# Optimization experiments

Measured on AMD Instinct MI355X. Metric: run time of the kernel, lower is better.

## Reference

```python
import jax, jax.numpy as jnp
import numpy as np

B, N, D, DEPTH = 1, 512, 128, 4


def mlp_apply(W, x):
    # W: (depth, d, d), x: (..., d). First layer has no activation, then silu before each matmul.
    x = x @ W[0]
    for i in range(1, DEPTH):
        x = jax.nn.silu(x) @ W[i]
    return x


def _binop(x, y):
    # linear recurrence combine: s_t = a_t * s_{t-1} + b_t
    a1, b1 = x
    a2, b2 = y
    return (a1 * a2, a2 * b1 + b2)


def setup_inputs() -> dict:
    key = jax.random.key(0)
    ks = jax.random.split(key, 7)
    s = 0.02  # scale for projection weights (torch Linear-like init magnitude)
    return {
        "seq": jax.random.normal(ks[0], (B, N, D), jnp.float32),
        "W_mem": jax.random.normal(ks[1], (DEPTH, D, D), jnp.float32) * (D ** -0.5),
        "W_q": jax.random.normal(ks[2], (D, D), jnp.float32) * s,
        "W_kv": jax.random.normal(ks[3], (D, 2 * D), jnp.float32) * s,
        "W_mom": jax.random.normal(ks[4], (D, 1), jnp.float32) * s,
        "W_step": jax.random.normal(ks[5], (D, 1), jnp.float32) * s,
        "W_decay": jax.random.normal(ks[6], (D, 1), jnp.float32) * s,
    }


def reference(seq, W_mem, W_q, W_kv, W_mom, W_step, W_decay):
    b, n, d = seq.shape
    # --- store_memories ---
    adaptive_lr = (seq @ W_step)[..., 0]            # (b, n)
    adaptive_mom = seq @ W_mom                      # (b, n, 1)
    decay = jax.nn.sigmoid(seq @ W_decay)           # (b, n, 1)

    kv = seq.reshape(b * n, d) @ W_kv               # (bn, 2d)
    keys, values = kv[:, :d], kv[:, d:]

    def loss_fn(W, k, v):
        pred = mlp_apply(W, k)                      # (d,)
        # (pred - v)^2 .mean(-1).sum() for a single sample == mean over d
        return jnp.mean((pred - v) ** 2)

    # per-sample meta-gradients wrt memory MLP weights
    losses, grads = jax.vmap(jax.value_and_grad(loss_fn, argnums=0), in_axes=(None, 0, 0))(W_mem, keys, values)
    grads = grads.reshape(b, n, DEPTH, d, d)
    surprise = grads * (-adaptive_lr)[..., None, None, None]   # (b,n,depth,d,d)

    # momentum_t = adaptive_mom_t * momentum_{t-1} + surprise_t  (assoc. scan over n)
    am = adaptive_mom[..., None, None]              # (b, n, 1, 1, 1)
    _, momentum = jax.lax.associative_scan(_binop, (am, surprise), axis=1)

    # update_t = (1 - decay_t) * update_{t-1} + momentum_t
    dec = (1.0 - decay)[..., None, None]            # (b, n, 1, 1, 1)
    _, updates = jax.lax.associative_scan(_binop, (dec, momentum), axis=1)

    # --- retrieve_memories with per-token updated weights ---
    q = (seq @ W_q).reshape(b * n, d)
    W_tok = (W_mem[None, None] + updates).reshape(b * n, DEPTH, d, d)
    retrieved = jax.vmap(mlp_apply)(W_tok, q).reshape(b, n, d)
    return retrieved
```

## Files before the change

kernel.cpp:

```cpp
#include <hip/hip_runtime.h>
#include <hip/hip_bf16.h>
#include <math.h>

#define N 512
#define NN (N*N)
#define D 128
#define DD (D*D)
#define ND (N*D)
#define LSTR 132
#define CSTR 36

__device__ __forceinline__ float sigmoidf_(float x) { return 1.f / (1.f + expf(-x)); }

__global__ void k_transpose(const float* __restrict__ W_mem, float* __restrict__ WT) {
    int idx = blockIdx.x * 256 + threadIdx.x;
    int l = idx / DD;
    int r = idx % DD;
    int i = r / D;
    int j = r % D;
    WT[idx] = W_mem[(l + 1) * DD + j * D + i];
}

__global__ __launch_bounds__(512) void k_phase1(
    const float* __restrict__ seq, const float* __restrict__ W_mem,
    const float* __restrict__ W_q, const float* __restrict__ W_kv,
    const float* __restrict__ W_mom, const float* __restrict__ W_step,
    const float* __restrict__ W_decay, const float* __restrict__ WT,
    float* __restrict__ Q, float* __restrict__ INS, float* __restrict__ ES,
    float* __restrict__ am, float* __restrict__ dec)
{
    __shared__ float s_seq[D], s_v[D], s_cur[D];
    __shared__ float s_h[4][D];
    __shared__ float s_part[4][D];
    __shared__ float s_p3[4][3][D];
    __shared__ float s_red[8];
    __shared__ float s_lr;

    const int t = blockIdx.x;
    const int tid = threadIdx.x;
    const int j = tid & 127;
    const int p = tid >> 7;
    const int i0 = p * 32;

    if (p == 0) s_seq[j] = seq[t * D + j];
    __syncthreads();

    float ps = 0.f;
    if (p == 1) ps = s_seq[j] * W_step[j];
    else if (p == 2) ps = s_seq[j] * W_mom[j];
    else if (p == 3) ps = s_seq[j] * W_decay[j];
#pragma unroll
    for (int off = 32; off > 0; off >>= 1) ps += __shfl_down(ps, off);
    if ((tid & 63) == 0) s_red[tid >> 6] = ps;
    __syncthreads();
    if (tid == 0) s_lr = s_red[2] + s_red[3];
    else if (tid == 1) am[t] = s_red[4] + s_red[5];
    else if (tid == 2) dec[t] = 1.f - sigmoidf_(s_red[6] + s_red[7]);

    float kp = 0.f, vp = 0.f, qp = 0.f;
#pragma unroll 8
    for (int ii = 0; ii < 32; ii++) {
        int i = i0 + ii;
        float si = s_seq[i];
        kp += si * W_kv[i * 256 + j];
        vp += si * W_kv[i * 256 + 128 + j];
        qp += si * W_q[i * 128 + j];
    }
    s_p3[p][0][j] = kp; s_p3[p][1][j] = vp; s_p3[p][2][j] = qp;
    __syncthreads();
    if (p == 0) {
        float kj = s_p3[0][0][j] + s_p3[1][0][j] + s_p3[2][0][j] + s_p3[3][0][j];
        s_cur[j] = kj;
        INS[t * D + j] = kj;
    } else if (p == 1) {
        s_v[j] = s_p3[0][1][j] + s_p3[1][1][j] + s_p3[2][1][j] + s_p3[3][1][j];
    } else if (p == 2) {
        Q[t * D + j] = s_p3[0][2][j] + s_p3[1][2][j] + s_p3[2][2][j] + s_p3[3][2][j];
    }
    __syncthreads();

    for (int l = 0; l < 4; l++) {
        const float* Wl = W_mem + l * DD;
        float yp = 0.f;
#pragma unroll 8
        for (int ii = 0; ii < 32; ii++) {
            int i = i0 + ii;
            yp += s_cur[i] * Wl[i * D + j];
        }
        s_part[p][j] = yp;
        __syncthreads();
        if (p == 0) {
            float y = s_part[0][j] + s_part[1][j] + s_part[2][j] + s_part[3][j];
            s_h[l][j] = y;
            if (l < 3) {
                float a = y * sigmoidf_(y);
                s_cur[j] = a;
                INS[(l + 1) * ND + t * D + j] = a;
            }
        }
        __syncthreads();
    }

    if (p == 0) {
        float e = -s_lr * (2.f / (float)D) * (s_h[3][j] - s_v[j]);
        ES[3 * ND + t * D + j] = e;
        s_cur[j] = e;
    }
    __syncthreads();

    for (int l = 3; l >= 1; l--) {
        const float* Wt = WT + (l - 1) * DD;
        float gp = 0.f;
#pragma unroll 8
        for (int ii = 0; ii < 32; ii++) {
            int i = i0 + ii;
            gp += s_cur[i] * Wt[i * D + j];
        }
        s_part[p][j] = gp;
        __syncthreads();
        if (p == 0) {
            float g = s_part[0][j] + s_part[1][j] + s_part[2][j] + s_part[3][j];
            float h = s_h[l - 1][j];
            float sg = sigmoidf_(h);
            float e2 = g * (sg * (1.f + h * (1.f - sg)));
            ES[(l - 1) * ND + t * D + j] = e2;
            s_cur[j] = e2;
        }
        __syncthreads();
    }
}

__global__ __launch_bounds__(512) void k_logscan(
    const float* __restrict__ am, const float* __restrict__ dec,
    double* __restrict__ LA, double* __restrict__ LDp, int* __restrict__ NC)
{
    __shared__ double sa[N], sd[N];
    __shared__ int sn[N];
    const int t = threadIdx.x;
    float a = am[t];
    float d = dec[t];
    sa[t] = log((double)fmaxf(fabsf(a), 1e-38f));
    sd[t] = log((double)fmaxf(d, 1e-38f));
    sn[t] = (a < 0.f) ? 1 : 0;
    __syncthreads();
    for (int off = 1; off < N; off <<= 1) {
        double va = 0.0, vd = 0.0; int vn = 0;
        if (t >= off) { va = sa[t - off]; vd = sd[t - off]; vn = sn[t - off]; }
        __syncthreads();
        sa[t] += va; sd[t] += vd; sn[t] += vn;
        __syncthreads();
    }
    LA[t] = sa[t]; LDp[t] = sd[t]; NC[t] = sn[t];
}

__global__ __launch_bounds__(256) void k_build(
    const double* __restrict__ LA, const double* __restrict__ LDp,
    const int* __restrict__ NC,
    float* __restrict__ Amat, float* __restrict__ Dmat)
{
    int idx = blockIdx.x * 256 + threadIdx.x;
    int u = idx >> 9;
    int s = idx & (N - 1);
    float va = 0.f, vd = 0.f;
    if (s <= u) {
        va = expf((float)(LA[u] - LA[s]));
        if ((NC[u] - NC[s]) & 1) va = -va;
        vd = expf((float)(LDp[u] - LDp[s]));
    }
    Amat[idx] = va;
    Dmat[idx] = vd;
}

__global__ __launch_bounds__(256) void k_betamm(
    const float* __restrict__ Dmat, const float* __restrict__ Amat,
    float* __restrict__ betaP)
{
    const int bs = blockIdx.x;
    const int bt = blockIdx.y;
    const int z  = blockIdx.z;
    if (bs > bt) return;
    const int span = bt - bs + 1;
    const int chunk = (span + 3) >> 2;
    const int kBeg = bs + z * chunk;
    const int kEnd = (kBeg + chunk < bt + 1) ? (kBeg + chunk) : (bt + 1);
    if (kBeg >= kEnd) return;

    __shared__ float sA[32 * 34];
    __shared__ float sDT[32 * 34];

    const int tid = threadIdx.x;
    const int tx = tid & 15;
    const int ty = tid >> 4;
    float acc00 = 0.f, acc01 = 0.f, acc10 = 0.f, acc11 = 0.f;

    for (int kt = kBeg; kt < kEnd; kt++) {
        for (int i = tid; i < 1024; i += 256) {
            int r = i >> 5, c = i & 31;
            sA[r * 34 + c]  = Amat[(kt * 32 + r) * N + bs * 32 + c];
            sDT[c * 34 + r] = Dmat[(bt * 32 + r) * N + kt * 32 + c];
        }
        __syncthreads();
#pragma unroll 8
        for (int k = 0; k < 32; k++) {
            float2 a = *(float2*)&sA[k * 34 + 2 * tx];
            float2 d = *(float2*)&sDT[k * 34 + 2 * ty];
            acc00 += d.x * a.x; acc01 += d.x * a.y;
            acc10 += d.y * a.x; acc11 += d.y * a.y;
        }
        __syncthreads();
    }
    float* bp = betaP + z * NN + (bt * 32 + 2 * ty) * N + bs * 32 + 2 * tx;
    *(float2*)bp       = make_float2(acc00, acc01);
    *(float2*)(bp + N) = make_float2(acc10, acc11);
}

__global__ __launch_bounds__(256) void k_betared(
    const float* __restrict__ betaP, float* __restrict__ beta)
{
    int idx4 = blockIdx.x * 256 + threadIdx.x;
    int t  = idx4 >> 7;
    int s0 = (idx4 & 127) * 4;
    int bt = t >> 5, bs = s0 >> 5;
    float4 v = make_float4(0.f, 0.f, 0.f, 0.f);
    if (bs <= bt) {
        int span = bt - bs + 1;
        int chunk = (span + 3) >> 2;
        int nz = (span + chunk - 1) / chunk;
        v = *(const float4*)(betaP + t * N + s0);
        for (int z = 1; z < nz; z++) {
            float4 u = *(const float4*)(betaP + z * NN + t * N + s0);
            v.x += u.x; v.y += u.y; v.z += u.z; v.w += u.w;
        }
    }
    *(float4*)(beta + t * N + s0) = v;
}

__global__ __launch_bounds__(256) void k_layer(
    const float* __restrict__ Xsrc, float* __restrict__ Pout,
    const float* __restrict__ Wl, const float* __restrict__ INSl,
    const float* __restrict__ ESl, const float* __restrict__ beta,
    int mode)
{
    const int r = blockIdx.x;
    const int z = blockIdx.y;
    const bool isW = (z == 8);
    if (!isW && 4 * z > r) return;
    const int t0 = r * 16;
    const int lane = threadIdx.x;

    __shared__ float sX[16 * LSTR];
    __shared__ float sI[32 * LSTR];
    __shared__ float sE[32 * LSTR];
    __shared__ float sc[16 * CSTR];

    const int nzs = (r >> 2) + 1;
#pragma unroll
    for (int i = 0; i < 2; i++) {
        int f4 = lane + 256 * i;
        int row = f4 >> 5, c4 = f4 & 31;
        float4 v = ((const float4*)(Xsrc + t0 * D))[f4];
        if (mode) {
            for (int zz = 1; zz < nzs; zz++) {
                float4 u = ((const float4*)(Xsrc + zz * ND + t0 * D))[f4];
                v.x += u.x; v.y += u.y; v.z += u.z; v.w += u.w;
            }
            float4 w = ((const float4*)(Xsrc + 8 * ND + t0 * D))[f4];
            v.x += w.x; v.y += w.y; v.z += w.z; v.w += w.w;
            v.x = v.x * sigmoidf_(v.x); v.y = v.y * sigmoidf_(v.y);
            v.z = v.z * sigmoidf_(v.z); v.w = v.w * sigmoidf_(v.w);
        }
        *(float4*)(sX + row * LSTR + c4 * 4) = v;
    }

    const int ti  = lane >> 4;
    const int q15 = lane & 15;
    const int j8  = q15 * 8;

    if (isW) {
        __syncthreads();
        float acc[8];
#pragma unroll
        for (int b = 0; b < 8; b++) acc[b] = 0.f;
#pragma unroll 4
        for (int k = 0; k < D; k++) {
            float4 w0 = *(const float4*)(Wl + k * D + j8);
            float4 w1 = *(const float4*)(Wl + k * D + j8 + 4);
            float xv = sX[ti * LSTR + k];
            acc[0] += xv * w0.x; acc[1] += xv * w0.y;
            acc[2] += xv * w0.z; acc[3] += xv * w0.w;
            acc[4] += xv * w1.x; acc[5] += xv * w1.y;
            acc[6] += xv * w1.z; acc[7] += xv * w1.w;
        }
        float* yp = Pout + 8 * ND + (t0 + ti) * D + j8;
        *(float4*)yp       = make_float4(acc[0], acc[1], acc[2], acc[3]);
        *(float4*)(yp + 4) = make_float4(acc[4], acc[5], acc[6], acc[7]);
        return;
    }

    const int si0 = q15 * 2;
    float acc[8];
#pragma unroll
    for (int b = 0; b < 8; b++) acc[b] = 0.f;

    for (int sub = 0; sub < 2; sub++) {
        const int s0 = z * 64 + sub * 32;
        __syncthreads();
#pragma unroll
        for (int i = 0; i < 4; i++) {
            int f4 = lane + 256 * i;
            int row = f4 >> 5, c4 = f4 & 31;
            float4 a = ((const float4*)(INSl + s0 * D))[f4];
            float4 b = ((const float4*)(ESl + s0 * D))[f4];
            *(float4*)(sI + row * LSTR + c4 * 4) = a;
            *(float4*)(sE + row * LSTR + c4 * 4) = b;
        }
        float b0 = beta[(t0 + ti) * N + s0 + si0];
        float b1 = beta[(t0 + ti) * N + s0 + si0 + 1];
        __syncthreads();

        float g0 = 0.f, g1 = 0.f;
#pragma unroll 8
        for (int k4 = 0; k4 < D; k4 += 4) {
            float4 a  = *(float4*)(sX + ti * LSTR + k4);
            float4 p0 = *(float4*)(sI + si0 * LSTR + k4);
            float4 p1 = *(float4*)(sI + (si0 + 1) * LSTR + k4);
            g0 += a.x * p0.x + a.y * p0.y + a.z * p0.z + a.w * p0.w;
            g1 += a.x * p1.x + a.y * p1.y + a.z * p1.z + a.w * p1.w;
        }
        sc[ti * CSTR + si0]     = g0 * b0;
        sc[ti * CSTR + si0 + 1] = g1 * b1;
        __syncthreads();

#pragma unroll 8
        for (int s = 0; s < 32; s++) {
            float cv = sc[ti * CSTR + s];
            float4 e0 = *(float4*)(sE + s * LSTR + j8);
            float4 e1 = *(float4*)(sE + s * LSTR + j8 + 4);
            acc[0] += cv * e0.x; acc[1] += cv * e0.y;
            acc[2] += cv * e0.z; acc[3] += cv * e0.w;
            acc[4] += cv * e1.x; acc[5] += cv * e1.y;
            acc[6] += cv * e1.z; acc[7] += cv * e1.w;
        }
    }

    float* yp = Pout + z * ND + (t0 + ti) * D + j8;
    *(float4*)yp       = make_float4(acc[0], acc[1], acc[2], acc[3]);
    *(float4*)(yp + 4) = make_float4(acc[4], acc[5], acc[6], acc[7]);
}

__global__ __launch_bounds__(256) void k_reduce(
    const float* __restrict__ P, float* __restrict__ out)
{
    int f4 = blockIdx.x * 256 + threadIdx.x;
    int t = f4 >> 5;
    int r = t >> 4;
    int nzs = (r >> 2) + 1;
    float4 v = ((const float4*)P)[f4];
    for (int zz = 1; zz < nzs; zz++) {
        float4 u = ((const float4*)(P + zz * ND))[f4];
        v.x += u.x; v.y += u.y; v.z += u.z; v.w += u.w;
    }
    float4 w = ((const float4*)(P + 8 * ND))[f4];
    v.x += w.x; v.y += w.y; v.z += w.z; v.w += w.w;
    ((float4*)out)[f4] = v;
}

extern "C" void kernel_launch(void* const* d_in, const int* in_sizes, int n_in,
                              void* d_out, int out_size, void* d_ws, size_t ws_size,
                              hipStream_t stream) {
    const float* seq     = (const float*)d_in[0];
    const float* W_mem   = (const float*)d_in[1];
    const float* W_q     = (const float*)d_in[2];
    const float* W_kv    = (const float*)d_in[3];
    const float* W_mom   = (const float*)d_in[4];
    const float* W_step  = (const float*)d_in[5];
    const float* W_decay = (const float*)d_in[6];
    float* out = (float*)d_out;

    float* ws   = (float*)d_ws;
    float* am   = ws;
    float* dec  = am + N;
    float* Q    = dec + N;
    float* INS  = Q + ND;
    float* ES   = INS + 4 * ND;
    float* beta = ES + 4 * ND;
    float* WT   = beta + NN;
    float* Amat = WT + 3 * DD;
    float* Dmat = Amat + NN;
    float* Pa   = Dmat + NN;
    float* Pb   = Pa + 9 * ND;
    double* LA  = (double*)(Pb + 9 * ND);
    double* LDp = LA + N;
    int* NC     = (int*)(LDp + N);
    float* betaP = Pa;

    k_transpose<<<192, 256, 0, stream>>>(W_mem, WT);
    k_phase1<<<N, 512, 0, stream>>>(seq, W_mem, W_q, W_kv, W_mom, W_step, W_decay,
                                    WT, Q, INS, ES, am, dec);
    k_logscan<<<1, N, 0, stream>>>(am, dec, LA, LDp, NC);
    k_build<<<(NN) / 256, 256, 0, stream>>>(LA, LDp, NC, Amat, Dmat);
    dim3 mmgrid(N / 32, N / 32, 4);
    k_betamm<<<mmgrid, 256, 0, stream>>>(Dmat, Amat, betaP);
    k_betared<<<NN / 4 / 256, 256, 0, stream>>>(betaP, beta);

    dim3 lgrid(32, 9);
    k_layer<<<lgrid, 256, 0, stream>>>(Q,  Pa, W_mem,          INS,          ES,          beta, 0);
    k_layer<<<lgrid, 256, 0, stream>>>(Pa, Pb, W_mem + DD,     INS + ND,     ES + ND,     beta, 1);
    k_layer<<<lgrid, 256, 0, stream>>>(Pb, Pa, W_mem + 2 * DD, INS + 2 * ND, ES + 2 * ND, beta, 1);
    k_layer<<<lgrid, 256, 0, stream>>>(Pa, Pb, W_mem + 3 * DD, INS + 3 * ND, ES + 3 * ND, beta, 1);
    k_reduce<<<64, 256, 0, stream>>>(Pb, out);
}
```

Measured before the change: 173.5 us.

## Fuse decay-matrix build into beta matmul, drop transpose, split layer s-range finer

Removes the separate transpose kernel by reading W_mem rows directly with float4 loads in the backward pass of phase1. The Amat/Dmat build kernel is fused into the beta matmul, which now computes the exp entries on the fly from the log-prefix sums, so the two N×N matrices are no longer written to and read back from memory. The layer kernel's source-token split goes from 8 slabs of 64 to 17 slabs of 32, which adds blocks for parallelism and removes the inner sub-loop. The cost is more partial-sum slabs for k_reduce and the next layer to read, and repeated exp evaluations inside the matmul tiles.

```diff
diff --git a/kernel.cpp b/kernel.cpp
--- a/kernel.cpp
+++ b/kernel.cpp
@@ -9,30 +9,22 @@
 #define ND (N*D)
 #define LSTR 132
 #define CSTR 36
+#define NSLAB 18
 
 __device__ __forceinline__ float sigmoidf_(float x) { return 1.f / (1.f + expf(-x)); }
-
-__global__ void k_transpose(const float* __restrict__ W_mem, float* __restrict__ WT) {
-    int idx = blockIdx.x * 256 + threadIdx.x;
-    int l = idx / DD;
-    int r = idx % DD;
-    int i = r / D;
-    int j = r % D;
-    WT[idx] = W_mem[(l + 1) * DD + j * D + i];
-}
 
 __global__ __launch_bounds__(512) void k_phase1(
     const float* __restrict__ seq, const float* __restrict__ W_mem,
     const float* __restrict__ W_q, const float* __restrict__ W_kv,
     const float* __restrict__ W_mom, const float* __restrict__ W_step,
-    const float* __restrict__ W_decay, const float* __restrict__ WT,
+    const float* __restrict__ W_decay,
     float* __restrict__ Q, float* __restrict__ INS, float* __restrict__ ES,
     float* __restrict__ am, float* __restrict__ dec)
 {
-    __shared__ float s_seq[D], s_v[D], s_cur[D];
-    __shared__ float s_h[4][D];
-    __shared__ float s_part[4][D];
-    __shared__ float s_p3[4][3][D];
+    __shared__ __align__(16) float s_seq[D], s_v[D], s_cur[D];
+    __shared__ __align__(16) float s_h[4][D];
+    __shared__ __align__(16) float s_part[4][D];
+    __shared__ __align__(16) float s_p3[4][3][D];
     __shared__ float s_red[8];
     __shared__ float s_lr;
 
@@ -109,12 +101,14 @@
     __syncthreads();
 
     for (int l = 3; l >= 1; l--) {
-        const float* Wt = WT + (l - 1) * DD;
+        const float4* wrow = (const float4*)(W_mem + l * DD + j * D + i0);
+        const float4* cur4 = (const float4*)(s_cur + i0);
         float gp = 0.f;
-#pragma unroll 8
-        for (int ii = 0; ii < 32; ii++) {
-            int i = i0 + ii;
-            gp += s_cur[i] * Wt[i * D + j];
+#pragma unroll
+        for (int ii = 0; ii < 8; ii++) {
+            float4 w = wrow[ii];
+            float4 c = cur4[ii];
+            gp += c.x * w.x + c.y * w.y + c.z * w.z + c.w * w.w;
         }
         s_part[p][j] = gp;
         __syncthreads();
@@ -153,27 +147,9 @@
     LA[t] = sa[t]; LDp[t] = sd[t]; NC[t] = sn[t];
 }
 
-__global__ __launch_bounds__(256) void k_build(
+__global__ __launch_bounds__(256) void k_betamm(
     const double* __restrict__ LA, const double* __restrict__ LDp,
-    const int* __restrict__ NC,
-    float* __restrict__ Amat, float* __restrict__ Dmat)
-{
-    int idx = blockIdx.x * 256 + threadIdx.x;
-    int u = idx >> 9;
-    int s = idx & (N - 1);
-    float va = 0.f, vd = 0.f;
-    if (s <= u) {
-        va = expf((float)(LA[u] - LA[s]));
-        if ((NC[u] - NC[s]) & 1) va = -va;
-        vd = expf((float)(LDp[u] - LDp[s]));
-    }
-    Amat[idx] = va;
-    Dmat[idx] = vd;
-}
-
-__global__ __launch_bounds__(256) void k_betamm(
-    const float* __restrict__ Dmat, const float* __restrict__ Amat,
-    float* __restrict__ betaP)
+    const int* __restrict__ NC, float* __restrict__ betaP)
 {
     const int bs = blockIdx.x;
     const int bt = blockIdx.y;
@@ -196,8 +172,15 @@
     for (int kt = kBeg; kt < kEnd; kt++) {
         for (int i = tid; i < 1024; i += 256) {
             int r = i >> 5, c = i & 31;
-            sA[r * 34 + c]  = Amat[(kt * 32 + r) * N + bs * 32 + c];
-            sDT[c * 34 + r] = Dmat[(bt * 32 + r) * N + kt * 32 + c];
+            int u2 = kt * 32 + r, s2 = bs * 32 + c;
+            float va = 0.f;
+            if (s2 <= u2) {
+                va = expf((float)(LA[u2] - LA[s2]));
+                if ((NC[u2] - NC[s2]) & 1) va = -va;
+            }
+            sA[r * 34 + c] = va;
+            int u1 = bt * 32 + r, s1 = kt * 32 + c;
+            sDT[c * 34 + r] = (s1 <= u1) ? expf((float)(LDp[u1] - LDp[s1])) : 0.f;
         }
         __syncthreads();
 #pragma unroll 8
@@ -243,17 +226,17 @@
 {
     const int r = blockIdx.x;
     const int z = blockIdx.y;
-    const bool isW = (z == 8);
-    if (!isW && 4 * z > r) return;
+    const bool isW = (z == 17);
+    if (!isW && 32 * z > 16 * r + 15) return;
     const int t0 = r * 16;
     const int lane = threadIdx.x;
 
-    __shared__ float sX[16 * LSTR];
-    __shared__ float sI[32 * LSTR];
-    __shared__ float sE[32 * LSTR];
-    __shared__ float sc[16 * CSTR];
-
-    const int nzs = (r >> 2) + 1;
+    __shared__ __align__(16) float sX[16 * LSTR];
+    __shared__ __align__(16) float sI[32 * LSTR];
+    __shared__ __align__(16) float sE[32 * LSTR];
+    __shared__ __align__(16) float sc[16 * CSTR];
+
+    const int nzs = (r >> 1) + 1;
 #pragma unroll
     for (int i = 0; i < 2; i++) {
         int f4 = lane + 256 * i;
@@ -264,7 +247,7 @@
                 float4 u = ((const float4*)(Xsrc + zz * ND + t0 * D))[f4];
                 v.x += u.x; v.y += u.y; v.z += u.z; v.w += u.w;
             }
-            float4 w = ((const float4*)(Xsrc + 8 * ND + t0 * D))[f4];
+            float4 w = ((const float4*)(Xsrc + 17 * ND + t0 * D))[f4];
             v.x += w.x; v.y += w.y; v.z += w.z; v.w += w.w;
             v.x = v.x * sigmoidf_(v.x); v.y = v.y * sigmoidf_(v.y);
             v.z = v.z * sigmoidf_(v.z); v.w = v.w * sigmoidf_(v.w);
@@ -291,58 +274,53 @@
             acc[4] += xv * w1.x; acc[5] += xv * w1.y;
             acc[6] += xv * w1.z; acc[7] += xv * w1.w;
         }
-        float* yp = Pout + 8 * ND + (t0 + ti) * D + j8;
+        float* yp = Pout + 17 * ND + (t0 + ti) * D + j8;
         *(float4*)yp       = make_float4(acc[0], acc[1], acc[2], acc[3]);
         *(float4*)(yp + 4) = make_float4(acc[4], acc[5], acc[6], acc[7]);
         return;
     }
 
+    const int s0 = z * 32;
+#pragma unroll
+    for (int i = 0; i < 4; i++) {
+        int f4 = lane + 256 * i;
+        int row = f4 >> 5, c4 = f4 & 31;
+        float4 a = ((const float4*)(INSl + s0 * D))[f4];
+        float4 b = ((const float4*)(ESl + s0 * D))[f4];
+        *(float4*)(sI + row * LSTR + c4 * 4) = a;
+        *(float4*)(sE + row * LSTR + c4 * 4) = b;
+    }
     const int si0 = q15 * 2;
+    float b0 = beta[(t0 + ti) * N + s0 + si0];
+    float b1 = beta[(t0 + ti) * N + s0 + si0 + 1];
+    __syncthreads();
+
+    float g0 = 0.f, g1 = 0.f;
+#pragma unroll 8
+    for (int k4 = 0; k4 < D; k4 += 4) {
+        float4 a  = *(float4*)(sX + ti * LSTR + k4);
+        float4 p0 = *(float4*)(sI + si0 * LSTR + k4);
+        float4 p1 = *(float4*)(sI + (si0 + 1) * LSTR + k4);
+        g0 += a.x * p0.x + a.y * p0.y + a.z * p0.z + a.w * p0.w;
+        g1 += a.x * p1.x + a.y * p1.y + a.z * p1.z + a.w * p1.w;
+    }
+    sc[ti * CSTR + si0]     = g0 * b0;
+    sc[ti * CSTR + si0 + 1] = g1 * b1;
+    __syncthreads();
+
     float acc[8];
 #pragma unroll
     for (int b = 0; b < 8; b++) acc[b] = 0.f;
-
-    for (int sub = 0; sub < 2; sub++) {
-        const int s0 = z * 64 + sub * 32;
-        __syncthreads();
-#pragma unroll
-        for (int i = 0; i < 4; i++) {
-            int f4 = lane + 256 * i;
-            int row = f4 >> 5, c4 = f4 & 31;
-            float4 a = ((const float4*)(INSl + s0 * D))[f4];
-            float4 b = ((const float4*)(ESl + s0 * D))[f4];
-            *(float4*)(sI + row * LSTR + c4 * 4) = a;
-            *(float4*)(sE + row * LSTR + c4 * 4) = b;
-        }
-        float b0 = beta[(t0 + ti) * N + s0 + si0];
-        float b1 = beta[(t0 + ti) * N + s0 + si0 + 1];
-        __syncthreads();
-
-        float g0 = 0.f, g1 = 0.f;
-#pragma unroll 8
-        for (int k4 = 0; k4 < D; k4 += 4) {
-            float4 a  = *(float4*)(sX + ti * LSTR + k4);
-            float4 p0 = *(float4*)(sI + si0 * LSTR + k4);
-            float4 p1 = *(float4*)(sI + (si0 + 1) * LSTR + k4);
-            g0 += a.x * p0.x + a.y * p0.y + a.z * p0.z + a.w * p0.w;
-            g1 += a.x * p1.x + a.y * p1.y + a.z * p1.z + a.w * p1.w;
-        }
-        sc[ti * CSTR + si0]     = g0 * b0;
-        sc[ti * CSTR + si0 + 1] = g1 * b1;
-        __syncthreads();
-
-#pragma unroll 8
-        for (int s = 0; s < 32; s++) {
-            float cv = sc[ti * CSTR + s];
-            float4 e0 = *(float4*)(sE + s * LSTR + j8);
-            float4 e1 = *(float4*)(sE + s * LSTR + j8 + 4);
-            acc[0] += cv * e0.x; acc[1] += cv * e0.y;
-            acc[2] += cv * e0.z; acc[3] += cv * e0.w;
-            acc[4] += cv * e1.x; acc[5] += cv * e1.y;
-            acc[6] += cv * e1.z; acc[7] += cv * e1.w;
-        }
-    }
-
+#pragma unroll 8
+    for (int s = 0; s < 32; s++) {
+        float cv = sc[ti * CSTR + s];
+        float4 e0 = *(float4*)(sE + s * LSTR + j8);
+        float4 e1 = *(float4*)(sE + s * LSTR + j8 + 4);
+        acc[0] += cv * e0.x; acc[1] += cv * e0.y;
+        acc[2] += cv * e0.z; acc[3] += cv * e0.w;
+        acc[4] += cv * e1.x; acc[5] += cv * e1.y;
+        acc[6] += cv * e1.z; acc[7] += cv * e1.w;
+    }
     float* yp = Pout + z * ND + (t0 + ti) * D + j8;
     *(float4*)yp       = make_float4(acc[0], acc[1], acc[2], acc[3]);
     *(float4*)(yp + 4) = make_float4(acc[4], acc[5], acc[6], acc[7]);
@@ -354,13 +332,13 @@
     int f4 = blockIdx.x * 256 + threadIdx.x;
     int t = f4 >> 5;
     int r = t >> 4;
-    int nzs = (r >> 2) + 1;
+    int nzs = (r >> 1) + 1;
     float4 v = ((const float4*)P)[f4];
     for (int zz = 1; zz < nzs; zz++) {
         float4 u = ((const float4*)(P + zz * ND))[f4];
         v.x += u.x; v.y += u.y; v.z += u.z; v.w += u.w;
     }
-    float4 w = ((const float4*)(P + 8 * ND))[f4];
+    float4 w = ((const float4*)(P + 17 * ND))[f4];
     v.x += w.x; v.y += w.y; v.z += w.z; v.w += w.w;
     ((float4*)out)[f4] = v;
 }
@@ -384,26 +362,21 @@
     float* INS  = Q + ND;
     float* ES   = INS + 4 * ND;
     float* beta = ES + 4 * ND;
-    float* WT   = beta + NN;
-    float* Amat = WT + 3 * DD;
-    float* Dmat = Amat + NN;
-    float* Pa   = Dmat + NN;
-    float* Pb   = Pa + 9 * ND;
-    double* LA  = (double*)(Pb + 9 * ND);
+    float* Pa   = beta + NN;
+    float* Pb   = Pa + NSLAB * ND;
+    double* LA  = (double*)(Pb + NSLAB * ND);
     double* LDp = LA + N;
     int* NC     = (int*)(LDp + N);
     float* betaP = Pa;
 
-    k_transpose<<<192, 256, 0, stream>>>(W_mem, WT);
     k_phase1<<<N, 512, 0, stream>>>(seq, W_mem, W_q, W_kv, W_mom, W_step, W_decay,
-                                    WT, Q, INS, ES, am, dec);
+                                    Q, INS, ES, am, dec);
     k_logscan<<<1, N, 0, stream>>>(am, dec, LA, LDp, NC);
-    k_build<<<(NN) / 256, 256, 0, stream>>>(LA, LDp, NC, Amat, Dmat);
     dim3 mmgrid(N / 32, N / 32, 4);
-    k_betamm<<<mmgrid, 256, 0, stream>>>(Dmat, Amat, betaP);
+    k_betamm<<<mmgrid, 256, 0, stream>>>(LA, LDp, NC, betaP);
     k_betared<<<NN / 4 / 256, 256, 0, stream>>>(betaP, beta);
 
-    dim3 lgrid(32, 9);
+    dim3 lgrid(32, 18);
     k_layer<<<lgrid, 256, 0, stream>>>(Q,  Pa, W_mem,          INS,          ES,          beta, 0);
     k_layer<<<lgrid, 256, 0, stream>>>(Pa, Pb, W_mem + DD,     INS + ND,     ES + ND,     beta, 1);
     k_layer<<<lgrid, 256, 0, stream>>>(Pb, Pa, W_mem + 2 * DD, INS + 2 * ND, ES + 2 * ND, beta, 1);
```

After: 202.3 us. 1.17x slower.

## Restructure k_layer to compute full 16x64 score tile up front with 2x2 register blocking

Applied to the files above, without the earlier changes.

The kernel now loads all 64 INS rows into shared memory at once and computes the whole 16x64 scaled score tile in one pass. Each thread handles a 2x2 block of (token, source) pairs, which reuses each shared-memory operand across two products. The second GEMM is re-mapped so each thread covers two token rows and four contiguous columns, letting each E float4 load feed both rows. This removes one barrier round and cuts redundant LDS traffic, at the cost of more shared memory per block (larger sI and sc), which may lower occupancy.

```diff
diff --git a/kernel.cpp b/kernel.cpp
--- a/kernel.cpp
+++ b/kernel.cpp
@@ -8,7 +8,7 @@
 #define DD (D*D)
 #define ND (N*D)
 #define LSTR 132
-#define CSTR 36
+#define CSTR 68
 
 __device__ __forceinline__ float sigmoidf_(float x) { return 1.f / (1.f + expf(-x)); }
 
@@ -248,10 +248,10 @@
     const int t0 = r * 16;
     const int lane = threadIdx.x;
 
-    __shared__ float sX[16 * LSTR];
-    __shared__ float sI[32 * LSTR];
-    __shared__ float sE[32 * LSTR];
-    __shared__ float sc[16 * CSTR];
+    __shared__ __align__(16) float sX[16 * LSTR];
+    __shared__ __align__(16) float sI[64 * LSTR];
+    __shared__ __align__(16) float sE[32 * LSTR];
+    __shared__ __align__(16) float sc[16 * CSTR];
 
     const int nzs = (r >> 2) + 1;
 #pragma unroll
@@ -272,12 +272,10 @@
         *(float4*)(sX + row * LSTR + c4 * 4) = v;
     }
 
-    const int ti  = lane >> 4;
-    const int q15 = lane & 15;
-    const int j8  = q15 * 8;
-
     if (isW) {
         __syncthreads();
+        const int ti  = lane >> 4;
+        const int j8  = (lane & 15) * 8;
         float acc[8];
 #pragma unroll
         for (int b = 0; b < 8; b++) acc[b] = 0.f;
@@ -297,55 +295,77 @@
         return;
     }
 
-    const int si0 = q15 * 2;
-    float acc[8];
-#pragma unroll
-    for (int b = 0; b < 8; b++) acc[b] = 0.f;
+    const int s0 = z * 64;
+
+#pragma unroll
+    for (int i = 0; i < 8; i++) {
+        int f4 = lane + 256 * i;
+        int row = f4 >> 5, c4 = f4 & 31;
+        float4 a = ((const float4*)(INSl + s0 * D))[f4];
+        *(float4*)(sI + row * LSTR + c4 * 4) = a;
+    }
+
+    const int rp = lane >> 5;
+    const int sp = lane & 31;
+    float b00 = beta[(t0 + 2 * rp) * N + s0 + sp];
+    float b01 = beta[(t0 + 2 * rp) * N + s0 + sp + 32];
+    float b10 = beta[(t0 + 2 * rp + 1) * N + s0 + sp];
+    float b11 = beta[(t0 + 2 * rp + 1) * N + s0 + sp + 32];
+    __syncthreads();
+
+    float g00 = 0.f, g01 = 0.f, g10 = 0.f, g11 = 0.f;
+#pragma unroll 8
+    for (int k4 = 0; k4 < D; k4 += 4) {
+        float4 a0 = *(float4*)(sX + (2 * rp) * LSTR + k4);
+        float4 a1 = *(float4*)(sX + (2 * rp + 1) * LSTR + k4);
+        float4 p0 = *(float4*)(sI + sp * LSTR + k4);
+        float4 p1 = *(float4*)(sI + (sp + 32) * LSTR + k4);
+        g00 += a0.x * p0.x + a0.y * p0.y + a0.z * p0.z + a0.w * p0.w;
+        g01 += a0.x * p1.x + a0.y * p1.y + a0.z * p1.z + a0.w * p1.w;
+        g10 += a1.x * p0.x + a1.y * p0.y + a1.z * p0.z + a1.w * p0.w;
+        g11 += a1.x * p1.x + a1.y * p1.y + a1.z * p1.z + a1.w * p1.w;
+    }
+    sc[(2 * rp) * CSTR + sp]          = g00 * b00;
+    sc[(2 * rp) * CSTR + sp + 32]     = g01 * b01;
+    sc[(2 * rp + 1) * CSTR + sp]      = g10 * b10;
+    sc[(2 * rp + 1) * CSTR + sp + 32] = g11 * b11;
+
+    const int tp = lane >> 5;
+    const int jc = (lane & 31) * 4;
+    float acc[2][4];
+#pragma unroll
+    for (int a = 0; a < 2; a++)
+#pragma unroll
+        for (int b = 0; b < 4; b++) acc[a][b] = 0.f;
 
     for (int sub = 0; sub < 2; sub++) {
-        const int s0 = z * 64 + sub * 32;
         __syncthreads();
 #pragma unroll
         for (int i = 0; i < 4; i++) {
             int f4 = lane + 256 * i;
             int row = f4 >> 5, c4 = f4 & 31;
-            float4 a = ((const float4*)(INSl + s0 * D))[f4];
-            float4 b = ((const float4*)(ESl + s0 * D))[f4];
-            *(float4*)(sI + row * LSTR + c4 * 4) = a;
+            float4 b = ((const float4*)(ESl + (s0 + sub * 32) * D))[f4];
             *(float4*)(sE + row * LSTR + c4 * 4) = b;
         }
-        float b0 = beta[(t0 + ti) * N + s0 + si0];
-        float b1 = beta[(t0 + ti) * N + s0 + si0 + 1];
-        __syncthreads();
-
-        float g0 = 0.f, g1 = 0.f;
-#pragma unroll 8
-        for (int k4 = 0; k4 < D; k4 += 4) {
-            float4 a  = *(float4*)(sX + ti * LSTR + k4);
-            float4 p0 = *(float4*)(sI + si0 * LSTR + k4);
-            float4 p1 = *(float4*)(sI + (si0 + 1) * LSTR + k4);
-            g0 += a.x * p0.x + a.y * p0.y + a.z * p0.z + a.w * p0.w;
-            g1 += a.x * p1.x + a.y * p1.y + a.z * p1.z + a.w * p1.w;
-        }
-        sc[ti * CSTR + si0]     = g0 * b0;
-        sc[ti * CSTR + si0 + 1] = g1 * b1;
-        __syncthreads();
-
+        __syncthreads();
+        const float* scp0 = sc + tp * CSTR + sub * 32;
+        const float* scp1 = sc + (tp + 8) * CSTR + sub * 32;
 #pragma unroll 8
         for (int s = 0; s < 32; s++) {
-            float cv = sc[ti * CSTR + s];
-            float4 e0 = *(float4*)(sE + s * LSTR + j8);
-            float4 e1 = *(float4*)(sE + s * LSTR + j8 + 4);
-            acc[0] += cv * e0.x; acc[1] += cv * e0.y;
-            acc[2] += cv * e0.z; acc[3] += cv * e0.w;
-            acc[4] += cv * e1.x; acc[5] += cv * e1.y;
-            acc[6] += cv * e1.z; acc[7] += cv * e1.w;
-        }
-    }
-
-    float* yp = Pout + z * ND + (t0 + ti) * D + j8;
-    *(float4*)yp       = make_float4(acc[0], acc[1], acc[2], acc[3]);
-    *(float4*)(yp + 4) = make_float4(acc[4], acc[5], acc[6], acc[7]);
+            float c0 = scp0[s];
+            float c1 = scp1[s];
+            float4 e = *(float4*)(sE + s * LSTR + jc);
+            acc[0][0] += c0 * e.x; acc[0][1] += c0 * e.y;
+            acc[0][2] += c0 * e.z; acc[0][3] += c0 * e.w;
+            acc[1][0] += c1 * e.x; acc[1][1] += c1 * e.y;
+            acc[1][2] += c1 * e.z; acc[1][3] += c1 * e.w;
+        }
+    }
+
+    float* yp0 = Pout + z * ND + (t0 + tp) * D + jc;
+    float* yp1 = Pout + z * ND + (t0 + tp + 8) * D + jc;
+    *(float4*)yp0 = make_float4(acc[0][0], acc[0][1], acc[0][2], acc[0][3]);
+    *(float4*)yp1 = make_float4(acc[1][0], acc[1][1], acc[1][2], acc[1][3]);
 }
 
 __global__ __launch_bounds__(256) void k_reduce(
```

Result: faster. 163.2 us (-6.0%).
